# Kernel tuning notes

Hardware: AMD Instinct MI355X
Metric: run time of the kernel (lower is better)

Reference implementation:

```python
import math
import jax, jax.numpy as jnp
import numpy as np

N_FREQS = 16
MAX_PERIOD = 4096.0
INJECTION_SCALE = 1.0


def setup_inputs() -> dict:
    key = jax.random.key(0)
    ks = jax.random.split(key, 5)
    B, L, D, K = 4, 8192, 1024, 2
    read_in = K * 2 * N_FREQS  # 64
    x = jax.random.normal(ks[0], (B, L, D), dtype=jnp.float32)
    # Linear weights stored as (in, out) so y = x @ W + b (== torch x @ W.T + b)
    inc_w = jax.random.normal(ks[1], (D, K), dtype=jnp.float32) * 0.02
    inc_b = jnp.full((K,), -2.0, dtype=jnp.float32)   # nn.init.constant_(inc_proj.bias, -2.0)
    reset_w = jax.random.normal(ks[2], (D, K), dtype=jnp.float32) * 0.02
    reset_b = jnp.full((K,), -5.0, dtype=jnp.float32)  # nn.init.constant_(reset_proj.bias, -5.0)
    read_w = jax.random.normal(ks[3], (read_in, D), dtype=jnp.float32) * 0.02
    read_b = jnp.zeros((D,), dtype=jnp.float32)
    return {"x": x, "inc_w": inc_w, "inc_b": inc_b, "reset_w": reset_w,
            "reset_b": reset_b, "read_w": read_w, "read_b": read_b}


def reference(x, inc_w, inc_b, reset_w, reset_b, read_w, read_b):
    # Gates from hidden state
    inc_logits = x @ inc_w + inc_b        # (B, L, K)
    reset_logits = x @ reset_w + reset_b  # (B, L, K)
    inc = jax.nn.sigmoid(inc_logits)
    keep = 1.0 - jax.nn.sigmoid(reset_logits)

    # Diagonal linear recurrence c[t] = keep[t]*c[t-1] + inc[t]
    # expressed as an associative scan over affine maps f(x) = k*x + i.
    def combine(left, right):
        kl, il = left
        kr, ir = right
        return (kl * kr, ir + kr * il)

    _, counters = jax.lax.associative_scan(combine, (keep, inc), axis=1)  # (B, L, K)

    # Sinusoidal readout: (B, L, K) -> (B, L, K*2*n_freqs)
    freqs = jnp.exp(jnp.linspace(0.0, math.log(MAX_PERIOD), N_FREQS)).astype(x.dtype)
    sc = counters[..., None] / freqs                       # (B, L, K, F)
    emb = jnp.concatenate([jnp.sin(sc), jnp.cos(sc)], -1)  # (B, L, K, 2F)
    B, L, K, _ = emb.shape
    emb = emb.reshape(B, L, K * 2 * N_FREQS)

    injection = INJECTION_SCALE * (emb @ read_w + read_b)  # (B, L, d_model)
    return injection, inc_logits, counters
```

## Files before the change

kernel.cpp:

```cpp
#include <hip/hip_runtime.h>

#define B_    4
#define L_    8192
#define D_    1024
#define ROWS_ 32768
#define NCH_  128

typedef __attribute__((ext_vector_type(8))) short  short8;
typedef __attribute__((ext_vector_type(4))) float  floatx4;

__device__ __forceinline__ unsigned short f2bf(float f){
  unsigned int u = __float_as_uint(f);
  u += 0x7fffu + ((u >> 16) & 1u);
  return (unsigned short)(u >> 16);
}

__global__ __launch_bounds__(512) void k_gates(
    const float* __restrict__ x,
    const float* __restrict__ inc_w, const float* __restrict__ inc_b,
    const float* __restrict__ reset_w, const float* __restrict__ reset_b,
    float* __restrict__ out_incl,
    float* __restrict__ cl, float* __restrict__ kc,
    float* __restrict__ sumP, float* __restrict__ sumQ)
{
  __shared__ float s_keep[128];
  __shared__ float s_inc[128];
  const int blk  = blockIdx.x;
  const int b    = blk >> 7;
  const int ch   = blk & 127;
  const int tid  = threadIdx.x;
  const int w    = tid >> 6;
  const int lane = tid & 63;

  float4 wia[4], wib[4], wra[4], wrb[4];
  #pragma unroll
  for (int i = 0; i < 4; ++i){
    const int d0 = i*256 + lane*4;
    const float4* pi = (const float4*)(inc_w + d0*2);
    wia[i] = pi[0]; wib[i] = pi[1];
    const float4* pr = (const float4*)(reset_w + d0*2);
    wra[i] = pr[0]; wrb[i] = pr[1];
  }
  const float bi0 = inc_b[0], bi1 = inc_b[1];
  const float br0 = reset_b[0], br1 = reset_b[1];

  const int row0 = b*L_ + ch*64 + w*8;
  float4 xc[4], xn[4];
  {
    const float4* xr = (const float4*)(x + (size_t)row0 * D_);
    #pragma unroll
    for (int i = 0; i < 4; ++i) xc[i] = xr[i*64 + lane];
  }
  #pragma unroll
  for (int r = 0; r < 8; ++r){
    if (r < 7){
      const float4* xr = (const float4*)(x + (size_t)(row0 + r + 1) * D_);
      #pragma unroll
      for (int i = 0; i < 4; ++i) xn[i] = xr[i*64 + lane];
    }
    float ai0=0.f, ai1=0.f, ar0=0.f, ar1=0.f;
    #pragma unroll
    for (int i = 0; i < 4; ++i){
      const float4 v = xc[i];
      ai0 += v.x*wia[i].x + v.y*wia[i].z + v.z*wib[i].x + v.w*wib[i].z;
      ai1 += v.x*wia[i].y + v.y*wia[i].w + v.z*wib[i].y + v.w*wib[i].w;
      ar0 += v.x*wra[i].x + v.y*wra[i].z + v.z*wrb[i].x + v.w*wrb[i].z;
      ar1 += v.x*wra[i].y + v.y*wra[i].w + v.z*wrb[i].y + v.w*wrb[i].w;
    }
    #pragma unroll
    for (int m = 1; m < 64; m <<= 1){
      ai0 += __shfl_xor(ai0, m);
      ai1 += __shfl_xor(ai1, m);
      ar0 += __shfl_xor(ar0, m);
      ar1 += __shfl_xor(ar1, m);
    }
    if (lane == 0){
      const int row = row0 + r;
      const float il0 = ai0 + bi0, il1 = ai1 + bi1;
      const float rl0 = ar0 + br0, rl1 = ar1 + br1;
      out_incl[(size_t)row*2 + 0] = il0;
      out_incl[(size_t)row*2 + 1] = il1;
      const int lr = w*8 + r;
      s_inc [lr*2+0] = 1.f / (1.f + __expf(-il0));
      s_inc [lr*2+1] = 1.f / (1.f + __expf(-il1));
      s_keep[lr*2+0] = 1.f - 1.f / (1.f + __expf(-rl0));
      s_keep[lr*2+1] = 1.f - 1.f / (1.f + __expf(-rl1));
    }
    #pragma unroll
    for (int i = 0; i < 4; ++i) xc[i] = xn[i];
  }
  __syncthreads();

  if (tid < 128){
    const int k = w;
    float P = s_keep[lane*2 + k];
    float Q = s_inc [lane*2 + k];
    #pragma unroll
    for (int ofs = 1; ofs < 64; ofs <<= 1){
      const float Pp = __shfl_up(P, ofs);
      const float Qp = __shfl_up(Q, ofs);
      if (lane >= ofs){ Q = Q + P * Qp; P = P * Pp; }
    }
    const int row = b*L_ + ch*64 + lane;
    cl[(size_t)row*2 + k] = Q;
    kc[(size_t)row*2 + k] = P;
    if (lane == 63){
      const int seq = b*2 + k;
      sumP[seq*NCH_ + ch] = P;
      sumQ[seq*NCH_ + ch] = Q;
    }
  }
}

__global__ __launch_bounds__(512) void k_scan2(
    const float* __restrict__ sumP, const float* __restrict__ sumQ,
    float* __restrict__ carry,
    const float* __restrict__ read_w, unsigned short* __restrict__ Bt)
{
  if (blockIdx.x == 0){
    const int tid  = threadIdx.x;
    const int seq  = tid >> 6;
    const int lane = tid & 63;
    const float* P0 = sumP + seq*NCH_;
    const float* Q0 = sumQ + seq*NCH_;
    float P = P0[lane], Q = Q0[lane];
    #pragma unroll
    for (int ofs = 1; ofs < 64; ofs <<= 1){
      const float Pp = __shfl_up(P, ofs);
      const float Qp = __shfl_up(Q, ofs);
      if (lane >= ofs){ Q = Q + P * Qp; P = P * Pp; }
    }
    if (lane == 0) carry[seq*NCH_ + 0] = 0.f;
    carry[seq*NCH_ + lane + 1] = Q;
    const float Pc = __shfl(P, 63);
    const float Qc = __shfl(Q, 63);
    float P2 = P0[64 + lane], Q2 = Q0[64 + lane];
    #pragma unroll
    for (int ofs = 1; ofs < 64; ofs <<= 1){
      const float Pp = __shfl_up(P2, ofs);
      const float Qp = __shfl_up(Q2, ofs);
      if (lane >= ofs){ Q2 = Q2 + P2 * Qp; P2 = P2 * Pp; }
    }
    Q2 = Q2 + P2 * Qc;
    if (lane < 63) carry[seq*NCH_ + 65 + lane] = Q2;
  } else {
    const int idx = (blockIdx.x - 1)*512 + threadIdx.x;
    const int n  = idx >> 6;
    const int kk = idx & 63;
    Bt[idx] = f2bf(read_w[(size_t)kk*D_ + n]);
  }
}

__global__ __launch_bounds__(256) void k_emb(
    const float* __restrict__ cl, const float* __restrict__ kc,
    const float* __restrict__ carry,
    float* __restrict__ out_cnt, unsigned short* __restrict__ emb)
{
  const int tid  = threadIdx.x;
  const int w    = tid >> 6;
  const int lane = tid & 63;
  const int gw   = blockIdx.x*4 + w;
  const int k    = lane >> 5;
  const int idx  = lane & 31;
  const int f    = idx & 15;
  const float invf = exp2f(-0.8f * (float)f);
  #pragma unroll
  for (int i = 0; i < 4; ++i){
    const int row = gw*4 + i;
    const int b   = row >> 13;
    const int l   = row & (L_ - 1);
    const int ch  = l >> 6;
    const float c0 = cl[(size_t)row*2+0] + kc[(size_t)row*2+0]*carry[(b*2+0)*NCH_ + ch];
    const float c1 = cl[(size_t)row*2+1] + kc[(size_t)row*2+1]*carry[(b*2+1)*NCH_ + ch];
    if (lane == 0) out_cnt[(size_t)row*2+0] = c0;
    if (lane == 1) out_cnt[(size_t)row*2+1] = c1;
    const float c  = k ? c1 : c0;
    const float sc = c * invf;
    float rev = sc * 0.15915494309189535f;
    rev -= floorf(rev);
    const float e = (idx < 16) ? __builtin_amdgcn_sinf(rev)
                               : __builtin_amdgcn_cosf(rev);
    emb[(size_t)row*64 + lane] = f2bf(e);
  }
}

__global__ __launch_bounds__(256) void k_gemm(
    const unsigned short* __restrict__ emb, const unsigned short* __restrict__ Bt,
    const float* __restrict__ read_b, float* __restrict__ out)
{
  const int tid  = threadIdx.x;
  const int w    = tid >> 6;
  const int lane = tid & 63;
  const int rb   = blockIdx.x >> 2;
  const int cb   = blockIdx.x & 3;
  const int rowBase = rb * 16;
  const int colBase = cb * 256 + w * 64;
  const int m    = lane & 15;
  const int quad = lane >> 4;

  const short8* ap = (const short8*)(emb + (size_t)(rowBase + m) * 64);
  const short8 a0 = ap[quad];
  const short8 a1 = ap[4 + quad];

  floatx4 acc[4] = {{0.f,0.f,0.f,0.f},{0.f,0.f,0.f,0.f},
                    {0.f,0.f,0.f,0.f},{0.f,0.f,0.f,0.f}};
  #pragma unroll
  for (int ct = 0; ct < 4; ++ct){
    const int n = colBase + ct*16 + m;
    const short8* bp = (const short8*)(Bt + (size_t)n * 64);
    const short8 b0 = bp[quad];
    const short8 b1 = bp[4 + quad];
    acc[ct] = __builtin_amdgcn_mfma_f32_16x16x32_bf16(a0, b0, acc[ct], 0, 0, 0);
    acc[ct] = __builtin_amdgcn_mfma_f32_16x16x32_bf16(a1, b1, acc[ct], 0, 0, 0);
  }
  #pragma unroll
  for (int ct = 0; ct < 4; ++ct){
    const int col  = colBase + ct*16 + m;
    const float bias = read_b[col];
    #pragma unroll
    for (int r = 0; r < 4; ++r){
      const int row = rowBase + quad*4 + r;
      out[(size_t)row*D_ + col] = acc[ct][r] + bias;
    }
  }
}

extern "C" void kernel_launch(void* const* d_in, const int* in_sizes, int n_in,
                              void* d_out, int out_size, void* d_ws, size_t ws_size,
                              hipStream_t stream) {
  const float* x       = (const float*)d_in[0];
  const float* inc_w   = (const float*)d_in[1];
  const float* inc_b   = (const float*)d_in[2];
  const float* reset_w = (const float*)d_in[3];
  const float* reset_b = (const float*)d_in[4];
  const float* read_w  = (const float*)d_in[5];
  const float* read_b  = (const float*)d_in[6];

  float* out      = (float*)d_out;
  float* out_incl = out + (size_t)ROWS_ * D_;
  float* out_cnt  = out_incl + ROWS_ * 2;

  char* ws = (char*)d_ws;
  float* cl    = (float*)(ws + 0);
  float* kc    = (float*)(ws + 262144);
  float* sumP  = (float*)(ws + 524288);
  float* sumQ  = (float*)(ws + 528384);
  float* carry = (float*)(ws + 532480);
  unsigned short* emb = (unsigned short*)(ws + 540672);
  unsigned short* Bt  = (unsigned short*)(ws + 540672 + 4194304);

  k_gates<<<dim3(512),  dim3(512), 0, stream>>>(x, inc_w, inc_b, reset_w, reset_b,
                                                out_incl, cl, kc, sumP, sumQ);
  k_scan2<<<dim3(129),  dim3(512), 0, stream>>>(sumP, sumQ, carry, read_w, Bt);
  k_emb  <<<dim3(2048), dim3(256), 0, stream>>>(cl, kc, carry, out_cnt, emb);
  k_gemm <<<dim3(8192), dim3(256), 0, stream>>>(emb, Bt, read_b, out);
}
```

Measured before the change: 274.7 us.

## Fuse sinusoidal embedding into readout GEMM and compute A fragments in registers

Measured after the change: 264.5 us. -3.7%, faster.

```diff
diff --git a/kernel.cpp b/kernel.cpp
--- a/kernel.cpp
+++ b/kernel.cpp
@@ -151,61 +151,53 @@
   }
 }
 
-__global__ __launch_bounds__(256) void k_emb(
+__global__ __launch_bounds__(256) void k_fused(
     const float* __restrict__ cl, const float* __restrict__ kc,
     const float* __restrict__ carry,
-    float* __restrict__ out_cnt, unsigned short* __restrict__ emb)
+    const unsigned short* __restrict__ Bt,
+    const float* __restrict__ read_b,
+    float* __restrict__ out_cnt, float* __restrict__ out)
 {
   const int tid  = threadIdx.x;
   const int w    = tid >> 6;
   const int lane = tid & 63;
-  const int gw   = blockIdx.x*4 + w;
-  const int k    = lane >> 5;
-  const int idx  = lane & 31;
-  const int f    = idx & 15;
-  const float invf = exp2f(-0.8f * (float)f);
-  #pragma unroll
-  for (int i = 0; i < 4; ++i){
-    const int row = gw*4 + i;
-    const int b   = row >> 13;
-    const int l   = row & (L_ - 1);
-    const int ch  = l >> 6;
-    const float c0 = cl[(size_t)row*2+0] + kc[(size_t)row*2+0]*carry[(b*2+0)*NCH_ + ch];
-    const float c1 = cl[(size_t)row*2+1] + kc[(size_t)row*2+1]*carry[(b*2+1)*NCH_ + ch];
-    if (lane == 0) out_cnt[(size_t)row*2+0] = c0;
-    if (lane == 1) out_cnt[(size_t)row*2+1] = c1;
-    const float c  = k ? c1 : c0;
-    const float sc = c * invf;
-    float rev = sc * 0.15915494309189535f;
-    rev -= floorf(rev);
-    const float e = (idx < 16) ? __builtin_amdgcn_sinf(rev)
-                               : __builtin_amdgcn_cosf(rev);
-    emb[(size_t)row*64 + lane] = f2bf(e);
-  }
-}
-
-__global__ __launch_bounds__(256) void k_gemm(
-    const unsigned short* __restrict__ emb, const unsigned short* __restrict__ Bt,
-    const float* __restrict__ read_b, float* __restrict__ out)
-{
-  const int tid  = threadIdx.x;
-  const int w    = tid >> 6;
-  const int lane = tid & 63;
-  const int rb   = blockIdx.x >> 2;
-  const int cb   = blockIdx.x & 3;
-  const int rowBase = rb * 16;
-  const int colBase = cb * 256 + w * 64;
+  const int rowBase = blockIdx.x * 16;
   const int m    = lane & 15;
   const int quad = lane >> 4;
 
-  const short8* ap = (const short8*)(emb + (size_t)(rowBase + m) * 64);
-  const short8 a0 = ap[quad];
-  const short8 a1 = ap[4 + quad];
-
-  floatx4 acc[4] = {{0.f,0.f,0.f,0.f},{0.f,0.f,0.f,0.f},
-                    {0.f,0.f,0.f,0.f},{0.f,0.f,0.f,0.f}};
-  #pragma unroll
-  for (int ct = 0; ct < 4; ++ct){
+  const int row = rowBase + m;
+  const int b   = row >> 13;
+  const int ch  = (row & (L_ - 1)) >> 6;
+  const float2 clv = *(const float2*)(cl + (size_t)row*2);
+  const float2 kcv = *(const float2*)(kc + (size_t)row*2);
+  const float c0 = clv.x + kcv.x * carry[(b*2+0)*NCH_ + ch];
+  const float c1 = clv.y + kcv.y * carry[(b*2+1)*NCH_ + ch];
+  if (w == 0 && lane < 16){
+    ((float2*)out_cnt)[row] = make_float2(c0, c1);
+  }
+
+  const float TWO_PI_INV = 0.15915494309189535f;
+  const float STEP = 0.5743491774985175f;
+  float invf = (quad & 1) ? 0.011841535573494211f  : 1.0f;
+  const bool use_cos = (quad >> 1) != 0;
+  short8 a0, a1;
+  #pragma unroll
+  for (int j = 0; j < 8; ++j){
+    float r0 = c0 * invf * TWO_PI_INV; r0 -= floorf(r0);
+    float r1 = c1 * invf * TWO_PI_INV; r1 -= floorf(r1);
+    const float e0 = use_cos ? __builtin_amdgcn_cosf(r0) : __builtin_amdgcn_sinf(r0);
+    const float e1 = use_cos ? __builtin_amdgcn_cosf(r1) : __builtin_amdgcn_sinf(r1);
+    a0[j] = (short)f2bf(e0);
+    a1[j] = (short)f2bf(e1);
+    invf *= STEP;
+  }
+
+  const int colBase = w * 256;
+  floatx4 acc[16];
+  #pragma unroll
+  for (int ct = 0; ct < 16; ++ct) acc[ct] = (floatx4){0.f,0.f,0.f,0.f};
+  #pragma unroll
+  for (int ct = 0; ct < 16; ++ct){
     const int n = colBase + ct*16 + m;
     const short8* bp = (const short8*)(Bt + (size_t)n * 64);
     const short8 b0 = bp[quad];
@@ -213,14 +205,15 @@
     acc[ct] = __builtin_amdgcn_mfma_f32_16x16x32_bf16(a0, b0, acc[ct], 0, 0, 0);
     acc[ct] = __builtin_amdgcn_mfma_f32_16x16x32_bf16(a1, b1, acc[ct], 0, 0, 0);
   }
-  #pragma unroll
-  for (int ct = 0; ct < 4; ++ct){
+
+  #pragma unroll
+  for (int ct = 0; ct < 16; ++ct){
     const int col  = colBase + ct*16 + m;
     const float bias = read_b[col];
     #pragma unroll
     for (int r = 0; r < 4; ++r){
-      const int row = rowBase + quad*4 + r;
-      out[(size_t)row*D_ + col] = acc[ct][r] + bias;
+      const int orow = rowBase + quad*4 + r;
+      out[(size_t)orow*D_ + col] = acc[ct][r] + bias;
     }
   }
 }
@@ -246,12 +239,11 @@
   float* sumP  = (float*)(ws + 524288);
   float* sumQ  = (float*)(ws + 528384);
   float* carry = (float*)(ws + 532480);
-  unsigned short* emb = (unsigned short*)(ws + 540672);
-  unsigned short* Bt  = (unsigned short*)(ws + 540672 + 4194304);
+  unsigned short* Bt  = (unsigned short*)(ws + 540672);
 
   k_gates<<<dim3(512),  dim3(512), 0, stream>>>(x, inc_w, inc_b, reset_w, reset_b,
                                                 out_incl, cl, kc, sumP, sumQ);
   k_scan2<<<dim3(129),  dim3(512), 0, stream>>>(sumP, sumQ, carry, read_w, Bt);
-  k_emb  <<<dim3(2048), dim3(256), 0, stream>>>(cl, kc, carry, out_cnt, emb);
-  k_gemm <<<dim3(8192), dim3(256), 0, stream>>>(emb, Bt, read_b, out);
-}
+  k_fused<<<dim3(2048), dim3(256), 0, stream>>>(cl, kc, carry, Bt, read_b,
+                                                out_cnt, out);
+}
```
